# Optimization experiments

Measured on AMD Instinct MI355X. Metric: run time of the kernel, lower is better.

## Reference

```python
import jax, jax.numpy as jnp
import numpy as np

LSTM = 256
NUM_CELLS = 5
BLOCKS = 6
TEMP = 5.0
TANH_C = 1.1


def setup_inputs() -> dict:
    key = jax.random.key(0)
    ks = jax.random.split(key, 8)
    s = 0.05  # small init so sigmoids/tanh stay in sane range
    return {
        "enc_w": jax.random.normal(ks[0], (5, LSTM), jnp.float32) * s,
        "w_ih": jax.random.normal(ks[1], (4 * LSTM, LSTM), jnp.float32) * s,
        "w_hh": jax.random.normal(ks[2], (4 * LSTM, LSTM), jnp.float32) * s,
        "b_ih": jax.random.normal(ks[3], (4 * LSTM,), jnp.float32) * s,
        "b_hh": jax.random.normal(ks[4], (4 * LSTM,), jnp.float32) * s,
        "w1": jax.random.normal(ks[5], (LSTM, LSTM), jnp.float32) * s,
        "w2": jax.random.normal(ks[6], (LSTM, LSTM), jnp.float32) * s,
        "v": jax.random.normal(ks[7], (LSTM,), jnp.float32) * s,
    }


def _lstm_cell(x, h, c, w_ih, w_hh, b_ih, b_hh):
    # torch.nn.LSTMCell gate order: i, f, g, o
    g = w_ih @ x + b_ih + w_hh @ h + b_hh  # [4*LSTM]
    i, f, gg, o = jnp.split(g, 4)
    i, f, o = jax.nn.sigmoid(i), jax.nn.sigmoid(f), jax.nn.sigmoid(o)
    c2 = f * c + i * jnp.tanh(gg)
    h2 = o * jnp.tanh(c2)
    return h2, c2


def _run_sampler(bkey, enc_w, w_ih, w_hh, b_ih, b_hh, w1, w2, v):
    zeros = jnp.zeros((LSTM,), jnp.float32)
    inputs = enc_w[0]  # encoder(0)
    anchors = []
    anchors_w1 = []
    prev_h = prev_c = zeros
    # first two layers: LSTM always fed zero state (faithful to source)
    for _ in range(2):
        prev_h, prev_c = _lstm_cell(inputs, zeros, zeros, w_ih, w_hh, b_ih, b_hh)
        anchors.append(zeros)
        anchors_w1.append(w1 @ prev_h)
    arc_seq, log_probs, entropies = [], [], []
    step = 0
    for layer_id in range(2, NUM_CELLS + 2):
        for _ in range(2):
            prev_h, prev_c = _lstm_cell(inputs, prev_h, prev_c, w_ih, w_hh, b_ih, b_hh)
            q = jnp.tanh(jnp.stack(anchors_w1[:layer_id]) + w2 @ prev_h)  # [layer_id, LSTM]
            logits = (q @ v) / TEMP  # [layer_id]
            logits = TANH_C * jnp.tanh(logits)
            skey = jax.random.fold_in(bkey, step); step += 1
            index = jax.random.categorical(skey, logits)
            lsm = jax.nn.log_softmax(logits)
            arc_seq.append(index)
            log_probs.append(-lsm[index])  # F.cross_entropy
            entropies.append(jax.lax.stop_gradient(-jnp.sum(lsm * jnp.exp(lsm))))
            inputs = jnp.stack(anchors[:layer_id])[index]
        prev_h, prev_c = _lstm_cell(inputs, prev_h, prev_c, w_ih, w_hh, b_ih, b_hh)
        anchors.append(prev_h)
        anchors_w1.append(w1 @ prev_h)
        inputs = enc_w[0]
    arc = jnp.stack(arc_seq)  # [2*NUM_CELLS] int
    return arc, sum(entropies), sum(log_probs), prev_c, prev_h


def reference(enc_w, w_ih, w_hh, b_ih, b_hh, w1, w2, v):
    key = jax.random.key(42)
    all_arc = []
    all_entropy = jnp.float32(0.0)
    all_log_prob = jnp.float32(0.0)
    c = h = None
    for b in range(BLOCKS):
        arc, ent, lp, c, h = _run_sampler(
            jax.random.fold_in(key, b), enc_w, w_ih, w_hh, b_ih, b_hh, w1, w2, v)
        all_arc.append(arc)
        all_entropy = all_entropy + ent
        all_log_prob = all_log_prob + lp
    return (jnp.stack(all_arc), all_log_prob, all_entropy, c[None, :], h[None, :])
```

## Files before the change

kernel.cpp:

```cpp
#include <hip/hip_runtime.h>
#include <stdint.h>


#define NBLK  6
#define PWG   8
#define THR   512
#define TINYF 1.17549435e-38f
#define HTAGB 0xC3B00000u
#define YTAGB 0xE1700000u
#define ITAGB 0xA5D00000u
#define DONE_MAGIC 0x444f4e45

typedef unsigned long long u64;
struct U2 { uint32_t x, y; };

#define W_DONE 0u
#define W_PART 32u
#define W_IDX  80u
#define W_HX   320u
#define W_YMB  24896u
#define W_NEED 221504u

#define S_READY 0u
#define S_DONE  192u
#define S_PART  224u
#define S_HP    320u
#define S_ACC   24896u
#define FXS     67108864.0f
#define READY_MAGIC 0x52454459

__device__ __forceinline__ U2 tf2x32(uint32_t k0, uint32_t k1,
                                     uint32_t c0, uint32_t c1) {
  uint32_t ks2 = k0 ^ k1 ^ 0x1BD11BDAu;
  uint32_t x0 = c0 + k0, x1 = c1 + k1;
#define TFR(r) { x0 += x1; x1 = (x1 << (r)) | (x1 >> (32 - (r))); x1 ^= x0; }
  TFR(13) TFR(15) TFR(26) TFR(6)   x0 += k1;  x1 += ks2 + 1u;
  TFR(17) TFR(29) TFR(16) TFR(24)  x0 += ks2; x1 += k0 + 2u;
  TFR(13) TFR(15) TFR(26) TFR(6)   x0 += k0;  x1 += k1 + 3u;
  TFR(17) TFR(29) TFR(16) TFR(24)  x0 += k1;  x1 += ks2 + 4u;
  TFR(13) TFR(15) TFR(26) TFR(6)   x0 += ks2; x1 += k0 + 5u;
#undef TFR
  U2 r; r.x = x0; r.y = x1; return r;
}

__device__ __forceinline__ float sigf(float x) {
  return 1.0f / (1.0f + expf(-x));
}
__device__ __forceinline__ void istore(int* p, int v) {
  __hip_atomic_store(p, v, __ATOMIC_RELAXED, __HIP_MEMORY_SCOPE_AGENT);
}
__device__ __forceinline__ int iload(const int* p) {
  return __hip_atomic_load(p, __ATOMIC_RELAXED, __HIP_MEMORY_SCOPE_AGENT);
}
__device__ __forceinline__ void hstore(u64* p, u64 v) {
  __hip_atomic_store(p, v, __ATOMIC_RELAXED, __HIP_MEMORY_SCOPE_AGENT);
}
__device__ __forceinline__ u64 hload(const u64* p) {
  return __hip_atomic_load(p, __ATOMIC_RELAXED, __HIP_MEMORY_SCOPE_AGENT);
}
__device__ __forceinline__ void fstore(float* p, float v) {
  __hip_atomic_store(p, v, __ATOMIC_RELAXED, __HIP_MEMORY_SCOPE_AGENT);
}
__device__ __forceinline__ float fload(const float* p) {
  return __hip_atomic_load(p, __ATOMIC_RELAXED, __HIP_MEMORY_SCOPE_AGENT);
}
__device__ __forceinline__ u64 pollw(const u64* p, uint32_t want) {
  u64 v;
  for (;;) {
    v = hload(p);
    if ((uint32_t)(v >> 32) == want) return v;
    __builtin_amdgcn_s_sleep(1);
  }
}

__global__ __launch_bounds__(THR, 2) void ctrl_v19(
    const float* __restrict__ enc_w,
    const float* __restrict__ wih,
    const float* __restrict__ whh,
    const float* __restrict__ b_ih,
    const float* __restrict__ b_hh,
    const float* __restrict__ w1,
    const float* __restrict__ w2,
    const float* __restrict__ vvec,
    unsigned char* __restrict__ ws,
    float* __restrict__ out) {

  const int b = blockIdx.x & 7;
  const int p = blockIdx.x >> 3;
  if (b >= NBLK) return;
  const int tid = threadIdx.x;

  int*   done = (int*)(ws + W_DONE);
  float* part = (float*)(ws + W_PART);
  int*   idxw = (int*)(ws + W_IDX);
  u64*   hx   = (u64*)(ws + W_HX);
  u64*   ymb  = (u64*)(ws + W_YMB);

  const int rl = tid & 127, s = tid >> 7;
  const int grow = (rl >> 5) * 256 + p * 32 + (rl & 31);
  const int k0 = s * 64;
  const int rr = tid & 255, ks = tid >> 8;
  const int cb = p * 32 + ks * 16;

  __shared__ __align__(16) float gateL[THR];
  __shared__ __align__(16) float hL[256], encL[256], vL[256];
  __shared__ __align__(16) float anchL[4][256];
  __shared__ __align__(16) float w2hS[256], aw1S[6][256];
  __shared__ float biasS[128], h2S[32];
  __shared__ float logitL[8];
  __shared__ int   selL;

  if (tid < 256) { encL[tid] = enc_w[tid]; vL[tid] = vvec[tid]; }
  if (tid < 128) {
    int r = (tid >> 5) * 256 + p * 32 + (tid & 31);
    biasS[tid] = b_ih[r] + b_hh[r];
  }

  float4 wihr[16], whhr[16];
  #pragma unroll
  for (int c = 0; c < 16; ++c) {
    wihr[c] = *(const float4*)(wih + grow * 256 + k0 + c * 4);
    whhr[c] = *(const float4*)(whh + grow * 256 + k0 + c * 4);
  }
  float w1c[16], w2c[16];
  #pragma unroll
  for (int j = 0; j < 16; ++j) {
    w1c[j] = w1[rr * 256 + cb + j];
    w2c[j] = w2[rr * 256 + cb + j];
  }
  __syncthreads();

  auto dotIH = [&](const float* x) {
    float a = 0.0f;
    #pragma unroll
    for (int c = 0; c < 16; ++c) {
      float4 xv = *(const float4*)(x + k0 + c * 4);
      float4 w = wihr[c];
      a += w.x * xv.x + w.y * xv.y + w.z * xv.z + w.w * xv.w;
    }
    return a;
  };
  auto dotHH = [&]() {
    float a = 0.0f;
    #pragma unroll
    for (int c = 0; c < 16; ++c) {
      float4 xv = *(const float4*)(hL + k0 + c * 4);
      float4 w = whhr[c];
      a += w.x * xv.x + w.y * xv.y + w.z * xv.z + w.w * xv.w;
    }
    return a;
  };

  const float encih = dotIH(encL);

  float cv = 0.0f;
  U2 bk = tf2x32(0u, 42u, 0u, (uint32_t)b);
  int k = 1, step = 0;
  float lpAcc = 0.0f, entAcc = 0.0f;

  auto cell = [&](float gacc, int mode, int aid, int cid) {
    gateL[tid] = gacc;
    __syncthreads();
    if (tid < 32) {
      float rs[4];
      #pragma unroll
      for (int g = 0; g < 4; ++g) {
        float ssum = 0.0f;
        #pragma unroll
        for (int j = 0; j < 4; ++j) ssum += gateL[j * 128 + g * 32 + tid];
        rs[g] = ssum + biasS[g * 32 + tid];
      }
      float gi = rs[0], gf = rs[1], gg2 = rs[2], go = rs[3];
      float c2 = sigf(gf) * cv + sigf(gi) * tanhf(gg2);
      float h2 = sigf(go) * tanhf(c2);
      cv = c2;
      h2S[tid] = h2;
      if (mode == 2) {
        if (b == NBLK - 1) { out[62 + p * 32 + tid] = cv; out[318 + p * 32 + tid] = h2; }
      } else {
        hstore(&hx[(k & 1) * 1536 + b * 256 + p * 32 + tid],
               ((u64)(HTAGB | (uint32_t)k) << 32) | (u64)__float_as_uint(h2));
      }
    }
    __syncthreads();
    if (mode == 2) return;

    {
      const float* wc = (mode == 1) ? w1c : w2c;
      float yp = 0.0f;
      #pragma unroll
      for (int j = 0; j < 16; ++j) yp += wc[j] * h2S[ks * 16 + j];
      gateL[tid] = yp;
    }
    __syncthreads();

    const uint32_t wantY = YTAGB | (uint32_t)k;
    const uint32_t wantH = HTAGB | (uint32_t)k;
    u64* ybase = ymb + (size_t)(k & 1) * 12288 + (size_t)b * 2048;
    if (tid < 256) {
      float yp2 = gateL[tid] + gateL[256 + tid];
      hstore(ybase + (size_t)p * 256 + tid,
             ((u64)wantY << 32) | (u64)__float_as_uint(yp2));
      u64 v = pollw(&hx[(k & 1) * 1536 + b * 256 + tid], wantH);
      float hv = __uint_as_float((uint32_t)v);
      hL[tid] = hv;
      if (mode == 1 && cid >= 0) anchL[cid][tid] = hv;
    } else if (p == 0) {
      const int e = tid - 256;
      const u64* bp = ybase + e;
      u64 w[8];
      for (;;) {
        #pragma unroll
        for (int q = 0; q < 8; ++q) w[q] = hload(bp + q * 256);
        uint32_t bad = 0u;
        #pragma unroll
        for (int q = 0; q < 8; ++q) bad |= ((uint32_t)(w[q] >> 32) ^ wantY);
        if (bad == 0u) break;
        __builtin_amdgcn_s_sleep(1);
      }
      float y = 0.0f;
      #pragma unroll
      for (int q = 0; q < 8; ++q) y += __uint_as_float((uint32_t)w[q]);
      if (mode == 1) aw1S[aid][e] = y; else w2hS[e] = y;
    }
    __syncthreads();
    ++k;
  };

  auto resolve = [&](int L) -> int {
    if (p == 0) {
      int wv = tid >> 6, lane = tid & 63;
      if (wv < L) {
        float a = 0.0f;
        #pragma unroll
        for (int j = 0; j < 4; ++j) {
          int kk = j * 64 + lane;
          a += tanhf(aw1S[wv][kk] + w2hS[kk]) * vL[kk];
        }
        a += __shfl_down(a, 32);
        a += __shfl_down(a, 16);
        a += __shfl_down(a, 8);
        a += __shfl_down(a, 4);
        a += __shfl_down(a, 2);
        a += __shfl_down(a, 1);
        if (lane == 0) logitL[wv] = a;
      }
      __syncthreads();
      if (tid < 64) {
        float lg = 0.0f, sgum = -1e30f;
        if (tid < L) {
          lg = 1.1f * tanhf(logitL[tid] * 0.2f);
          U2 sk = tf2x32(bk.x, bk.y, 0u, (uint32_t)step);
          U2 r2 = tf2x32(sk.x, sk.y, 0u, (uint32_t)tid);
          uint32_t bits = r2.x ^ r2.y;
          float u = __uint_as_float((bits >> 9) | 0x3f800000u) - 1.0f;
          u = fmaxf(TINYF, u + TINYF);
          sgum = lg - logf(-logf(u));
        }
        int bi = 0;
        float best = __shfl(sgum, 0, 64);
        for (int j = 1; j < L; ++j) {
          float sj = __shfl(sgum, j, 64);
          if (sj > best) { best = sj; bi = j; }
        }
        float mx = __shfl(lg, 0, 64);
        for (int j = 1; j < L; ++j) mx = fmaxf(mx, __shfl(lg, j, 64));
        float se = 0.0f;
        for (int j = 0; j < L; ++j) se += expf(__shfl(lg, j, 64) - mx);
        float lse = logf(se);
        float lgbi = __shfl(lg, bi, 64);
        float es = 0.0f;
        for (int j = 0; j < L; ++j) {
          float l = __shfl(lg, j, 64) - mx - lse;
          es += l * expf(l);
        }
        if (tid == 0) {
          lpAcc += -(lgbi - mx - lse);
          entAcc += -es;
          selL = bi;
          out[b * 10 + step] = (float)bi;
          istore(&idxw[b * 10 + step],
                 (int)(ITAGB | ((uint32_t)step << 4) | (uint32_t)bi));
        }
      }
      __syncthreads();
    } else {
      if (tid == 0) {
        const uint32_t want = ITAGB | ((uint32_t)step << 4);
        for (;;) {
          uint32_t v = (uint32_t)iload(&idxw[b * 10 + step]);
          if ((v & 0xFFFFFFF0u) == want) { selL = (int)(v & 15u); break; }
          __builtin_amdgcn_s_sleep(1);
        }
      }
      __syncthreads();
    }
    step++;
    return selL;
  };

  cell(encih, 1, 0, -1);
  if (p == 0) {
    if (tid < 256) aw1S[1][tid] = aw1S[0][tid];
    __syncthreads();
  }

  for (int L = 2; L <= 6; ++L) {
    { float hh = dotHH(); cell(encih + hh, 0, 0, -1); }
    {
      int s1; float hh;
      if (p == 0) { s1 = resolve(L); hh = dotHH(); }
      else        { hh = dotHH(); s1 = resolve(L); }
      float a = (s1 >= 2) ? dotIH(&anchL[s1 - 2][0]) : 0.0f;
      cell(a + hh, 0, 0, -1);
    }
    {
      int s2; float hh;
      if (p == 0) { s2 = resolve(L); hh = dotHH(); }
      else        { hh = dotHH(); s2 = resolve(L); }
      float a = (s2 >= 2) ? dotIH(&anchL[s2 - 2][0]) : 0.0f;
      if (L < 6) cell(a + hh, 1, L, L - 2);
      else       cell(a + hh, 2, 0, -1);
    }
  }

  if (p == 0 && tid == 0) {
    fstore(&part[2 * b], lpAcc);
    fstore(&part[2 * b + 1], entAcc);
    __builtin_amdgcn_s_waitcnt(0);
    istore(&done[b], DONE_MAGIC);
    if (b == NBLK - 1) {
      float lp = 0.0f, en = 0.0f;
      for (int j = 0; j < NBLK; ++j) {
        while (iload(&done[j]) != DONE_MAGIC) __builtin_amdgcn_s_sleep(1);
        lp += fload(&part[2 * j]);
        en += fload(&part[2 * j + 1]);
      }
      out[60] = lp;
      out[61] = en;
    }
  }
}

__global__ __launch_bounds__(1024) void ctrl_small(
    const float* __restrict__ enc_w,
    const float* __restrict__ wih,
    const float* __restrict__ whh,
    const float* __restrict__ b_ih,
    const float* __restrict__ b_hh,
    const float* __restrict__ w1,
    const float* __restrict__ w2,
    const float* __restrict__ vvec,
    unsigned char* __restrict__ ws,
    float* __restrict__ out) {

  const int b = blockIdx.x & 7;
  const int p = blockIdx.x >> 3;
  if (b >= NBLK) return;
  const int tid = threadIdx.x;

  int*   ready = (int*)(ws + S_READY);
  int*   done  = (int*)(ws + S_DONE);
  float* part  = (float*)(ws + S_PART);
  u64*   hp    = (u64*)(ws + S_HP);
  int*   acc   = (int*)(ws + S_ACC);

  const int rl = tid >> 3, s = tid & 7;
  const int g = rl >> 5, el = rl & 31;
  const int row = g * 256 + p * 32 + el;
  const int k0 = s * 32;
  const int rr = tid & 255, ks = tid >> 8;

  __shared__ __align__(16) float hL[256], encL[256], vL[256];
  __shared__ __align__(16) float anchL[4][256];
  __shared__ __align__(16) float partL[1024];
  __shared__ __align__(16) float w2hS[256], aw1S[6][256];
  __shared__ float rowSumL[128], biasS[128], h2S[32];
  __shared__ float logitL[8];
  __shared__ int   selL;

  if (tid < 256) { encL[tid] = enc_w[tid]; vL[tid] = vvec[tid]; }
  if (tid < 128) {
    int gg = tid >> 5, ee = tid & 31, r = gg * 256 + p * 32 + ee;
    biasS[tid] = b_ih[r] + b_hh[r];
  }

  float4 wihr[8], whhr[8];
  #pragma unroll
  for (int c = 0; c < 8; ++c) {
    int cc = (c + s) & 7;
    wihr[c] = *(const float4*)(wih + row * 256 + k0 + cc * 4);
    whhr[c] = *(const float4*)(whh + row * 256 + k0 + cc * 4);
  }
  float w1c[8], w2c[8];
  #pragma unroll
  for (int j = 0; j < 8; ++j) {
    w1c[j] = w1[rr * 256 + p * 32 + ks * 8 + j];
    w2c[j] = w2[rr * 256 + p * 32 + ks * 8 + j];
  }

  if (tid < 32) istore(&acc[1 * (NBLK * 256) + b * 256 + p * 32 + tid], 0);
  __syncthreads();
  if (tid == 0) istore(&ready[b * 8 + p], READY_MAGIC);
  if (tid < 8) {
    while (iload(&ready[b * 8 + tid]) != READY_MAGIC)
      __builtin_amdgcn_s_sleep(1);
  }
  __syncthreads();

  auto dotIH = [&](const float* x) {
    float a = 0.0f;
    #pragma unroll
    for (int c = 0; c < 8; ++c) {
      int cc = (c + s) & 7;
      float4 xv = *(const float4*)(x + k0 + cc * 4);
      float4 w = wihr[c];
      a += w.x * xv.x + w.y * xv.y + w.z * xv.z + w.w * xv.w;
    }
    return a;
  };
  auto dotHH = [&]() {
    float a = 0.0f;
    #pragma unroll
    for (int c = 0; c < 8; ++c) {
      int cc = (c + s) & 7;
      float4 xv = *(const float4*)(hL + k0 + cc * 4);
      float4 w = whhr[c];
      a += w.x * xv.x + w.y * xv.y + w.z * xv.z + w.w * xv.w;
    }
    return a;
  };

  const float encih = dotIH(encL);
  float cv = 0.0f;
  U2 bk = tf2x32(0u, 42u, 0u, (uint32_t)b);
  int k = 1, step = 0;
  float lpAcc = 0.0f, entAcc = 0.0f;

  auto cell = [&](float gacc, int mode, int aid, int cid) {
    partL[tid] = gacc;
    __syncthreads();
    if (tid < 128) {
      float ssum = 0.0f;
      #pragma unroll
      for (int j = 0; j < 8; ++j) ssum += partL[tid * 8 + j];
      rowSumL[tid] = ssum + biasS[tid];
    }
    __syncthreads();
    if (tid < 32) {
      float gi = rowSumL[tid],       gf = rowSumL[32 + tid];
      float gg2 = rowSumL[64 + tid], go = rowSumL[96 + tid];
      float c2 = sigf(gf) * cv + sigf(gi) * tanhf(gg2);
      float h2 = sigf(go) * tanhf(c2);
      cv = c2;
      h2S[tid] = h2;
      if (mode == 2 && b == NBLK - 1) {
        out[62 + p * 32 + tid] = cv;
        out[318 + p * 32 + tid] = h2;
      }
    }
    __syncthreads();
    if (mode == 2) return;
    {
      const float* wc = (mode == 1) ? w1c : w2c;
      float yp = 0.0f;
      #pragma unroll
      for (int j = 0; j < 8; ++j) yp += wc[j] * h2S[ks * 8 + j];
      atomicAdd(&acc[(k % 3) * (NBLK * 256) + b * 256 + rr],
                __float2int_rn(yp * FXS));
      if (tid < 32)
        istore(&acc[((k + 1) % 3) * (NBLK * 256) + b * 256 + p * 32 + tid], 0);
    }
    __syncthreads();
    if (tid < 32) {
      u64 pk = ((u64)(uint32_t)k << 32) | (u64)__float_as_uint(h2S[tid]);
      hstore(&hp[(k & 1) * (NBLK * 256) + b * 256 + p * 32 + tid], pk);
    }
    if (tid < 256) {
      u64 v;
      const u64* src = &hp[(k & 1) * (NBLK * 256) + b * 256 + tid];
      while ((int)(hload(src) >> 32) != k) __builtin_amdgcn_s_sleep(1);
      v = hload(src);
      float hv = __uint_as_float((uint32_t)v);
      hL[tid] = hv;
      if (mode == 1 && cid >= 0) anchL[cid][tid] = hv;
    }
    __syncthreads();
    if (tid < 256) {
      int iv = iload(&acc[(k % 3) * (NBLK * 256) + b * 256 + tid]);
      float f = (float)((double)iv * (1.0 / 67108864.0));
      if (mode == 1) aw1S[aid][tid] = f; else w2hS[tid] = f;
    }
    __syncthreads();
    ++k;
  };

  auto sample = [&](int L) -> int {
    int wv = tid >> 6, lane = tid & 63;
    if (wv < L) {
      float a = 0.0f;
      #pragma unroll
      for (int j = 0; j < 4; ++j) {
        int kk = lane * 4 + j;
        a += tanhf(aw1S[wv][kk] + w2hS[kk]) * vL[kk];
      }
      a += __shfl_down(a, 32);
      a += __shfl_down(a, 16);
      a += __shfl_down(a, 8);
      a += __shfl_down(a, 4);
      a += __shfl_down(a, 2);
      a += __shfl_down(a, 1);
      if (lane == 0) logitL[wv] = a;
    }
    __syncthreads();
    if (tid < 64) {
      float lg = 0.0f, sgum = -1e30f;
      if (tid < L) {
        lg = 1.1f * tanhf(logitL[tid] * 0.2f);
        U2 sk = tf2x32(bk.x, bk.y, 0u, (uint32_t)step);
        U2 r2 = tf2x32(sk.x, sk.y, 0u, (uint32_t)tid);
        uint32_t bits = r2.x ^ r2.y;
        float u = __uint_as_float((bits >> 9) | 0x3f800000u) - 1.0f;
        u = fmaxf(TINYF, u + TINYF);
        sgum = lg - logf(-logf(u));
      }
      int bi = 0;
      float best = __shfl(sgum, 0, 64);
      for (int j = 1; j < L; ++j) {
        float sj = __shfl(sgum, j, 64);
        if (sj > best) { best = sj; bi = j; }
      }
      float mx = __shfl(lg, 0, 64);
      for (int j = 1; j < L; ++j) mx = fmaxf(mx, __shfl(lg, j, 64));
      float se = 0.0f;
      for (int j = 0; j < L; ++j) se += expf(__shfl(lg, j, 64) - mx);
      float lse = logf(se);
      float lgbi = __shfl(lg, bi, 64);
      float es = 0.0f;
      for (int j = 0; j < L; ++j) {
        float l = __shfl(lg, j, 64) - mx - lse;
        es += l * expf(l);
      }
      if (tid == 0) {
        lpAcc += -(lgbi - mx - lse);
        entAcc += -es;
        selL = bi;
        if (p == 0) out[b * 10 + step] = (float)bi;
      }
    }
    __syncthreads();
    step++;
    return selL;
  };

  cell(encih, 1, 0, -1);
  if (tid < 256) aw1S[1][tid] = aw1S[0][tid];
  __syncthreads();
  for (int L = 2; L <= 6; ++L) {
    cell(encih + dotHH(), 0, 0, -1);
    int s1v = sample(L);
    {
      float a = (s1v >= 2) ? dotIH(&anchL[s1v - 2][0]) : 0.0f;
      cell(a + dotHH(), 0, 0, -1);
    }
    int s2v = sample(L);
    {
      float a = (s2v >= 2) ? dotIH(&anchL[s2v - 2][0]) : 0.0f;
      if (L < 6) cell(a + dotHH(), 1, L, L - 2);
      else       cell(a + dotHH(), 2, 0, -1);
    }
  }
  if (p == 0 && tid == 0) {
    fstore(&part[2 * b], lpAcc);
    fstore(&part[2 * b + 1], entAcc);
    __builtin_amdgcn_s_waitcnt(0);
    istore(&done[b], DONE_MAGIC);
    if (b == NBLK - 1) {
      float lp = 0.0f, en = 0.0f;
      for (int j = 0; j < NBLK; ++j) {
        while (iload(&done[j]) != DONE_MAGIC) __builtin_amdgcn_s_sleep(1);
        lp += fload(&part[2 * j]);
        en += fload(&part[2 * j + 1]);
      }
      out[60] = lp;
      out[61] = en;
    }
  }
}

extern "C" void kernel_launch(void* const* d_in, const int* in_sizes, int n_in,
                              void* d_out, int out_size, void* d_ws, size_t ws_size,
                              hipStream_t stream) {
  const float* enc = (const float*)d_in[0];
  const float* wih = (const float*)d_in[1];
  const float* whh = (const float*)d_in[2];
  const float* bih = (const float*)d_in[3];
  const float* bhh = (const float*)d_in[4];
  const float* w1  = (const float*)d_in[5];
  const float* w2  = (const float*)d_in[6];
  const float* v   = (const float*)d_in[7];
  unsigned char* ws = (unsigned char*)d_ws;
  float* out = (float*)d_out;

  if (ws_size >= W_NEED) {
    ctrl_v19<<<dim3(64), dim3(THR), 0, stream>>>(
        enc, wih, whh, bih, bhh, w1, w2, v, ws, out);
  } else {
    ctrl_small<<<dim3(64), dim3(1024), 0, stream>>>(
        enc, wih, whh, bih, bhh, w1, w2, v, ws, out);
  }
}
```

Before: 146.8 us.

## Fuse attention sampling into the cell's y-gather warps using LDS counters

In the partition-0 workgroup, the attention logits and Gumbel sampling now run inside the cell's gather phase. The four gather waves sync with each other through workgroup-scope LDS atomic counters instead of two full-workgroup barriers in a separate resolve step. Partition 0 then reads the selected index directly from shared memory, and the final partial-sum write moves to thread 256, which now owns the accumulators. This shortens the serial critical path per sampling step, at the cost of spin-waiting on LDS counters and more fragile ordering between waves.

After: 157.4 us. 7.2% more time.

```diff
diff --git a/kernel.cpp b/kernel.cpp
--- a/kernel.cpp
+++ b/kernel.cpp
@@ -73,7 +73,7 @@
   }
 }
 
-__global__ __launch_bounds__(THR, 2) void ctrl_v19(
+__global__ __launch_bounds__(THR, 2) void ctrl_v20(
     const float* __restrict__ enc_w,
     const float* __restrict__ wih,
     const float* __restrict__ whh,
@@ -109,12 +109,14 @@
   __shared__ float biasS[128], h2S[32];
   __shared__ float logitL[8];
   __shared__ int   selL;
+  __shared__ int   upC1, upC2;
 
   if (tid < 256) { encL[tid] = enc_w[tid]; vL[tid] = vvec[tid]; }
   if (tid < 128) {
     int r = (tid >> 5) * 256 + p * 32 + (tid & 31);
     biasS[tid] = b_ih[r] + b_hh[r];
   }
+  if (tid == 0) { upC1 = 0; upC2 = 0; }
 
   float4 wihr[16], whhr[16];
   #pragma unroll
@@ -156,9 +158,10 @@
   float cv = 0.0f;
   U2 bk = tf2x32(0u, 42u, 0u, (uint32_t)b);
   int k = 1, step = 0;
+  int upT1 = 0, upT2 = 0;
   float lpAcc = 0.0f, entAcc = 0.0f;
 
-  auto cell = [&](float gacc, int mode, int aid, int cid) {
+  auto cell = [&](float gacc, int mode, int aid, int cid, int sampL) {
     gateL[tid] = gacc;
     __syncthreads();
     if (tid < 32) {
@@ -222,109 +225,123 @@
       #pragma unroll
       for (int q = 0; q < 8; ++q) y += __uint_as_float((uint32_t)w[q]);
       if (mode == 1) aw1S[aid][e] = y; else w2hS[e] = y;
-    }
-    __syncthreads();
+
+      if (sampL > 0) {
+        asm volatile("s_waitcnt lgkmcnt(0)" ::: "memory");
+        if ((tid & 63) == 0)
+          __hip_atomic_fetch_add(&upC1, 1, __ATOMIC_RELEASE,
+                                 __HIP_MEMORY_SCOPE_WORKGROUP);
+        upT1 += 4;
+        while (__hip_atomic_load(&upC1, __ATOMIC_ACQUIRE,
+                                 __HIP_MEMORY_SCOPE_WORKGROUP) < upT1) {}
+        const int uw = e >> 6, lane = tid & 63;
+        for (int wv = uw; wv < sampL; wv += 4) {
+          float a = 0.0f;
+          #pragma unroll
+          for (int j = 0; j < 4; ++j) {
+            int kk = j * 64 + lane;
+            a += tanhf(aw1S[wv][kk] + w2hS[kk]) * vL[kk];
+          }
+          a += __shfl_down(a, 32);
+          a += __shfl_down(a, 16);
+          a += __shfl_down(a, 8);
+          a += __shfl_down(a, 4);
+          a += __shfl_down(a, 2);
+          a += __shfl_down(a, 1);
+          if (lane == 0) logitL[wv] = a;
+        }
+        asm volatile("s_waitcnt lgkmcnt(0)" ::: "memory");
+        if ((tid & 63) == 0)
+          __hip_atomic_fetch_add(&upC2, 1, __ATOMIC_RELEASE,
+                                 __HIP_MEMORY_SCOPE_WORKGROUP);
+        upT2 += 4;
+        while (__hip_atomic_load(&upC2, __ATOMIC_ACQUIRE,
+                                 __HIP_MEMORY_SCOPE_WORKGROUP) < upT2) {}
+        if (uw == 0) {
+          float lg = 0.0f, sgum = -1e30f;
+          if (lane < sampL) {
+            lg = 1.1f * tanhf(logitL[lane] * 0.2f);
+            U2 sk = tf2x32(bk.x, bk.y, 0u, (uint32_t)step);
+            U2 r2 = tf2x32(sk.x, sk.y, 0u, (uint32_t)lane);
+            uint32_t bits = r2.x ^ r2.y;
+            float u = __uint_as_float((bits >> 9) | 0x3f800000u) - 1.0f;
+            u = fmaxf(TINYF, u + TINYF);
+            sgum = lg - logf(-logf(u));
+          }
+          int bi = 0;
+          float best = __shfl(sgum, 0, 64);
+          for (int j = 1; j < sampL; ++j) {
+            float sj = __shfl(sgum, j, 64);
+            if (sj > best) { best = sj; bi = j; }
+          }
+          float mx = __shfl(lg, 0, 64);
+          for (int j = 1; j < sampL; ++j) mx = fmaxf(mx, __shfl(lg, j, 64));
+          float se = 0.0f;
+          for (int j = 0; j < sampL; ++j) se += expf(__shfl(lg, j, 64) - mx);
+          float lse = logf(se);
+          float lgbi = __shfl(lg, bi, 64);
+          float es = 0.0f;
+          for (int j = 0; j < sampL; ++j) {
+            float l = __shfl(lg, j, 64) - mx - lse;
+            es += l * expf(l);
+          }
+          if (lane == 0) {
+            lpAcc += -(lgbi - mx - lse);
+            entAcc += -es;
+            selL = bi;
+            out[b * 10 + step] = (float)bi;
+            istore(&idxw[b * 10 + step],
+                   (int)(ITAGB | ((uint32_t)step << 4) | (uint32_t)bi));
+          }
+        }
+      }
+    }
+    __syncthreads();
+    if (sampL > 0 && p == 0) ++step;
     ++k;
   };
 
   auto resolve = [&](int L) -> int {
-    if (p == 0) {
-      int wv = tid >> 6, lane = tid & 63;
-      if (wv < L) {
-        float a = 0.0f;
-        #pragma unroll
-        for (int j = 0; j < 4; ++j) {
-          int kk = j * 64 + lane;
-          a += tanhf(aw1S[wv][kk] + w2hS[kk]) * vL[kk];
-        }
-        a += __shfl_down(a, 32);
-        a += __shfl_down(a, 16);
-        a += __shfl_down(a, 8);
-        a += __shfl_down(a, 4);
-        a += __shfl_down(a, 2);
-        a += __shfl_down(a, 1);
-        if (lane == 0) logitL[wv] = a;
-      }
-      __syncthreads();
-      if (tid < 64) {
-        float lg = 0.0f, sgum = -1e30f;
-        if (tid < L) {
-          lg = 1.1f * tanhf(logitL[tid] * 0.2f);
-          U2 sk = tf2x32(bk.x, bk.y, 0u, (uint32_t)step);
-          U2 r2 = tf2x32(sk.x, sk.y, 0u, (uint32_t)tid);
-          uint32_t bits = r2.x ^ r2.y;
-          float u = __uint_as_float((bits >> 9) | 0x3f800000u) - 1.0f;
-          u = fmaxf(TINYF, u + TINYF);
-          sgum = lg - logf(-logf(u));
-        }
-        int bi = 0;
-        float best = __shfl(sgum, 0, 64);
-        for (int j = 1; j < L; ++j) {
-          float sj = __shfl(sgum, j, 64);
-          if (sj > best) { best = sj; bi = j; }
-        }
-        float mx = __shfl(lg, 0, 64);
-        for (int j = 1; j < L; ++j) mx = fmaxf(mx, __shfl(lg, j, 64));
-        float se = 0.0f;
-        for (int j = 0; j < L; ++j) se += expf(__shfl(lg, j, 64) - mx);
-        float lse = logf(se);
-        float lgbi = __shfl(lg, bi, 64);
-        float es = 0.0f;
-        for (int j = 0; j < L; ++j) {
-          float l = __shfl(lg, j, 64) - mx - lse;
-          es += l * expf(l);
-        }
-        if (tid == 0) {
-          lpAcc += -(lgbi - mx - lse);
-          entAcc += -es;
-          selL = bi;
-          out[b * 10 + step] = (float)bi;
-          istore(&idxw[b * 10 + step],
-                 (int)(ITAGB | ((uint32_t)step << 4) | (uint32_t)bi));
-        }
-      }
-      __syncthreads();
-    } else {
-      if (tid == 0) {
-        const uint32_t want = ITAGB | ((uint32_t)step << 4);
-        for (;;) {
-          uint32_t v = (uint32_t)iload(&idxw[b * 10 + step]);
-          if ((v & 0xFFFFFFF0u) == want) { selL = (int)(v & 15u); break; }
-          __builtin_amdgcn_s_sleep(1);
-        }
-      }
-      __syncthreads();
-    }
+    (void)L;
+    if (tid == 0) {
+      const uint32_t want = ITAGB | ((uint32_t)step << 4);
+      for (;;) {
+        uint32_t v = (uint32_t)iload(&idxw[b * 10 + step]);
+        if ((v & 0xFFFFFFF0u) == want) { selL = (int)(v & 15u); break; }
+        __builtin_amdgcn_s_sleep(1);
+      }
+    }
+    __syncthreads();
     step++;
     return selL;
   };
 
-  cell(encih, 1, 0, -1);
+  cell(encih, 1, 0, -1, 0);
   if (p == 0) {
     if (tid < 256) aw1S[1][tid] = aw1S[0][tid];
     __syncthreads();
   }
 
   for (int L = 2; L <= 6; ++L) {
-    { float hh = dotHH(); cell(encih + hh, 0, 0, -1); }
+    { float hh = dotHH(); cell(encih + hh, 0, 0, -1, L); }
     {
       int s1; float hh;
-      if (p == 0) { s1 = resolve(L); hh = dotHH(); }
+      if (p == 0) { s1 = selL; hh = dotHH(); }
       else        { hh = dotHH(); s1 = resolve(L); }
       float a = (s1 >= 2) ? dotIH(&anchL[s1 - 2][0]) : 0.0f;
-      cell(a + hh, 0, 0, -1);
+      cell(a + hh, 0, 0, -1, L);
     }
     {
       int s2; float hh;
-      if (p == 0) { s2 = resolve(L); hh = dotHH(); }
+      if (p == 0) { s2 = selL; hh = dotHH(); }
       else        { hh = dotHH(); s2 = resolve(L); }
       float a = (s2 >= 2) ? dotIH(&anchL[s2 - 2][0]) : 0.0f;
-      if (L < 6) cell(a + hh, 1, L, L - 2);
-      else       cell(a + hh, 2, 0, -1);
-    }
-  }
-
-  if (p == 0 && tid == 0) {
+      if (L < 6) cell(a + hh, 1, L, L - 2, 0);
+      else       cell(a + hh, 2, 0, -1, 0);
+    }
+  }
+
+  if (p == 0 && tid == 256) {
     fstore(&part[2 * b], lpAcc);
     fstore(&part[2 * b + 1], entAcc);
     __builtin_amdgcn_s_waitcnt(0);
@@ -603,7 +620,7 @@
   float* out = (float*)d_out;
 
   if (ws_size >= W_NEED) {
-    ctrl_v19<<<dim3(64), dim3(THR), 0, stream>>>(
+    ctrl_v20<<<dim3(64), dim3(THR), 0, stream>>>(
         enc, wih, whh, bih, bhh, w1, w2, v, ws, out);
   } else {
     ctrl_small<<<dim3(64), dim3(1024), 0, stream>>>(
```
